# Kernel tuning notes

Hardware: AMD Instinct MI355X
Metric: run time of the kernel (lower is better)

## Reference

```python
import jax, jax.numpy as jnp
import numpy as np
import math

T = 4096          # num tokens (== context_window_len)
IN_SIZE = 2048    # model dim
HEAD_SIZE = 128   # per-head dim


def setup_inputs() -> dict:
    key = jax.random.key(0)
    kx, kq, kk, kv = jax.random.split(key, 4)
    scale = 1.0 / math.sqrt(IN_SIZE)
    x = jax.random.normal(kx, (T, IN_SIZE), dtype=jnp.float32)
    # eqx.nn.Linear(in, out) weight has shape [out, in], applied as W @ x
    Wq = jax.random.normal(kq, (HEAD_SIZE, IN_SIZE), dtype=jnp.float32) * scale
    Wk = jax.random.normal(kk, (HEAD_SIZE, IN_SIZE), dtype=jnp.float32) * scale
    Wv = jax.random.normal(kv, (HEAD_SIZE, IN_SIZE), dtype=jnp.float32) * scale
    return {"x": x, "Wq": Wq, "Wk": Wk, "Wv": Wv}


def reference(x, Wq, Wk, Wv):
    # q, k, v: [T, head_size]
    q = x @ Wq.T
    k = x @ Wk.T
    v = x @ Wv.T
    # scores: [T, T]
    scores = (q @ k.T) / math.sqrt(HEAD_SIZE)
    num_toks = x.shape[0]
    # causal mask: True above the diagonal (masked out)
    causal_mask = ~jnp.tril(jnp.ones((num_toks, num_toks), dtype=bool))
    masked = jnp.where(causal_mask, -jnp.inf, scores)
    attn = jax.nn.softmax(masked, axis=-1)
    return attn @ v
```

## Files before the change

kernel.cpp:

```cpp
#include <hip/hip_runtime.h>
#include <hip/hip_bf16.h>

#define T_TOK 4096
#define D_IN  2048
#define HS    128
#define CKV   4
#define NCH   16

typedef unsigned short u16;
typedef __attribute__((ext_vector_type(8))) __bf16 bf16x8;
typedef __attribute__((ext_vector_type(4))) float f32x4;
typedef __attribute__((ext_vector_type(4))) unsigned short us4;
typedef __attribute__((ext_vector_type(8))) unsigned short us8;

#define GLOBAL_AS __attribute__((address_space(1)))
#define LDS_AS    __attribute__((address_space(3)))

__device__ __forceinline__ void async_ld16(const void* g, void* l) {
  __builtin_amdgcn_global_load_lds((GLOBAL_AS void*)(void*)g, (LDS_AS void*)l, 16, 0, 0);
}

__device__ __forceinline__ u16 f2bf(float v) {
  return __builtin_bit_cast(u16, __float2bfloat16(v));
}

__device__ __forceinline__ void conv_body(const u16* in, u16* out, int n,
                                          int* flag, int write_flag,
                                          int blk, int tid) {
  __shared__ int sflag;
  if (tid < 64) {
    int cnt = 0;
#pragma unroll
    for (int j = 0; j < 8; j++) {
      u16 v = in[(tid * 8 + j) * 2];
      cnt += (((v >> 7) & 0xFF) >= 0xBF) ? 1 : 0;
    }
#pragma unroll
    for (int off = 1; off < 64; off <<= 1) cnt += __shfl_xor(cnt, off);
    if (tid == 0) sflag = (cnt > 8) ? 1 : 0;
  }
  __syncthreads();
  const bool isf32 = (sflag != 0);
  if (tid == 0 && write_flag && blk == 0) *flag = isf32 ? 1 : 0;
  const size_t base = ((size_t)blk * 256 + tid) * 8;
  if (base >= (size_t)n) return;
  if (isf32) {
    const float* f = (const float*)in;
    us4 a, b;
#pragma unroll
    for (int j = 0; j < 4; j++) a[j] = f2bf(f[base + j]);
#pragma unroll
    for (int j = 0; j < 4; j++) b[j] = f2bf(f[base + 4 + j]);
    *(us4*)(out + base) = a;
    *(us4*)(out + base + 4) = b;
  } else {
    *(us8*)(out + base) = *(const us8*)(in + base);
  }
}

__global__ __launch_bounds__(256) void conv_kernel(
    const u16* __restrict__ in, u16* __restrict__ out, int n,
    int* __restrict__ flag) {
  conv_body(in, out, n, flag, 1, blockIdx.x, threadIdx.x);
}

__global__ __launch_bounds__(256) void conv3_kernel(
    const u16* __restrict__ w0, const u16* __restrict__ w1,
    const u16* __restrict__ w2, u16* __restrict__ o0,
    u16* __restrict__ o1, u16* __restrict__ o2) {
  const int mat = blockIdx.x >> 7;
  const int blk = blockIdx.x & 127;
  const u16* in = (mat == 0) ? w0 : ((mat == 1) ? w1 : w2);
  u16* out = (mat == 0) ? o0 : ((mat == 1) ? o1 : o2);
  conv_body(in, out, HS * D_IN, nullptr, 0, blk, threadIdx.x);
}

__global__ __launch_bounds__(256, 2) void qkv_kernel(
    const u16* __restrict__ x, const u16* __restrict__ Wq,
    const u16* __restrict__ Wk, const u16* __restrict__ Wv,
    u16* __restrict__ Q, u16* __restrict__ K, u16* __restrict__ Vt)
{
  __shared__ __align__(16) u16 As[2][64 * 64];
  __shared__ __align__(16) u16 Bs[2][128 * 64];

  const int mat = blockIdx.y;
  const u16* W = (mat == 0) ? Wq : ((mat == 1) ? Wk : Wv);
  const int mtile = blockIdx.x;
  const int tid = threadIdx.x;
  const int wv = tid >> 6, lane = tid & 63, l15 = lane & 15, quad = lane >> 4;
  const int row0 = mtile * 64;

  f32x4 acc[8];
#pragma unroll
  for (int i = 0; i < 8; i++) acc[i] = (f32x4)0.0f;

  auto stage = [&](int k0, int buf) {
#pragma unroll
    for (int j = 0; j < 2; j++) {
      int s = (wv * 2 + j) * 64 + lane;
      int r = s >> 3, cs = s & 7, c = cs ^ (r & 7);
      async_ld16(x + (size_t)(row0 + r) * D_IN + k0 + c * 8,
                 (char*)As[buf] + (size_t)(wv * 2 + j) * 1024);
    }
#pragma unroll
    for (int j = 0; j < 4; j++) {
      int s = (wv * 4 + j) * 64 + lane;
      int n = s >> 3, cs = s & 7, c = cs ^ (n & 7);
      async_ld16(W + (size_t)n * D_IN + k0 + c * 8,
                 (char*)Bs[buf] + (size_t)(wv * 4 + j) * 1024);
    }
  };

  stage(0, 0);
  for (int kt = 0; kt < 32; kt++) {
    const int cur = kt & 1;
    __syncthreads();
    if (kt < 31) stage((kt + 1) * 64, 1 - cur);
#pragma unroll
    for (int kc = 0; kc < 2; kc++) {
      const int rA = 16 * wv + l15;
      const int cl = kc * 4 + quad;
      bf16x8 a = *(const bf16x8*)((const char*)As[cur] + (rA * 8 + (cl ^ (rA & 7))) * 16);
#pragma unroll
      for (int nt = 0; nt < 8; nt++) {
        int n = 16 * nt + l15;
        bf16x8 b = *(const bf16x8*)((const char*)Bs[cur] + (n * 8 + (cl ^ (n & 7))) * 16);
        acc[nt] = __builtin_amdgcn_mfma_f32_16x16x32_bf16(a, b, acc[nt], 0, 0, 0);
      }
    }
  }

  if (mat < 2) {
    u16* out = (mat == 0) ? Q : K;
#pragma unroll
    for (int nt = 0; nt < 8; nt++)
#pragma unroll
      for (int r = 0; r < 4; r++) {
        int m = row0 + 16 * wv + quad * 4 + r;
        int n = 16 * nt + l15;
        out[(size_t)m * HS + n] = f2bf(acc[nt][r]);
      }
  } else {
#pragma unroll
    for (int nt = 0; nt < 8; nt++) {
      int n = 16 * nt + l15;
      int mb = row0 + 16 * wv + quad * 4;
      us4 pk;
#pragma unroll
      for (int r = 0; r < 4; r++) pk[r] = f2bf(acc[nt][r]);
      *(us4*)(Vt + (size_t)n * T_TOK + mb) = pk;
    }
  }
}

__global__ __launch_bounds__(256, 2) void attn_split_kernel(
    const u16* __restrict__ Q, const u16* __restrict__ Kg,
    const u16* __restrict__ Vt, float* __restrict__ Opart,
    float* __restrict__ mstat, float* __restrict__ lstat)
{
  __shared__ __align__(16) u16 Ks[2][64 * 128];
  __shared__ __align__(16) u16 Vs[2][128 * 64];
  __shared__ __align__(16) u16 Ps[4 * 16 * 64];

  const int qtile = 63 - (int)blockIdx.x;
  const int ch = blockIdx.y;
  if (4 * ch > qtile) return;
  const int t0 = 4 * ch;
  const int nsteps = min(CKV, qtile + 1 - t0);
  const int q0 = qtile * 64;
  const int slot = 64 * ch - 2 * ch * (ch - 1) + (qtile - 4 * ch);

  const int tid = threadIdx.x;
  const int wv = tid >> 6, lane = tid & 63, l15 = lane & 15, quad = lane >> 4;

  bf16x8 qf[4];
#pragma unroll
  for (int kc = 0; kc < 4; kc++)
    qf[kc] = *(const bf16x8*)(Q + (size_t)(q0 + 16 * wv + l15) * HS + kc * 32 + quad * 8);

  f32x4 o[8];
#pragma unroll
  for (int i = 0; i < 8; i++) o[i] = (f32x4)0.0f;
  float mrun[4], lrun[4];
#pragma unroll
  for (int r = 0; r < 4; r++) { mrun[r] = -1e30f; lrun[r] = 0.0f; }

  const float sc = 0.12752761571239668f;

  auto stage = [&](int t, int buf) {
#pragma unroll
    for (int j = 0; j < 4; j++) {
      int s = (wv * 4 + j) * 64 + lane;
      int n = s >> 4, cs = s & 15, c = cs ^ (n & 7);
      async_ld16(Kg + (size_t)(t * 64 + n) * HS + c * 8,
                 (char*)Ks[buf] + (size_t)(wv * 4 + j) * 1024);
    }
#pragma unroll
    for (int j = 0; j < 4; j++) {
      int s = (wv * 4 + j) * 64 + lane;
      int vr = s >> 3, cs = s & 7, c = cs ^ (vr & 7);
      async_ld16(Vt + (size_t)vr * T_TOK + t * 64 + c * 8,
                 (char*)Vs[buf] + (size_t)(wv * 4 + j) * 1024);
    }
  };

  stage(t0, 0);
  for (int i = 0; i < nsteps; i++) {
    const int cur = i & 1;
    const int t = t0 + i;
    __syncthreads();
    if (i + 1 < nsteps) stage(t + 1, 1 - cur);

    f32x4 sacc[4];
#pragma unroll
    for (int nt = 0; nt < 4; nt++) sacc[nt] = (f32x4)0.0f;
#pragma unroll
    for (int kc = 0; kc < 4; kc++) {
      const int cl = kc * 4 + quad;
#pragma unroll
      for (int nt = 0; nt < 4; nt++) {
        int n = 16 * nt + l15;
        bf16x8 b = *(const bf16x8*)((const char*)Ks[cur] + (n * 16 + (cl ^ (n & 7))) * 16);
        sacc[nt] = __builtin_amdgcn_mfma_f32_16x16x32_bf16(qf[kc], b, sacc[nt], 0, 0, 0);
      }
    }

    float s2[4][4];
    const bool diag = (t == qtile);
#pragma unroll
    for (int nt = 0; nt < 4; nt++)
#pragma unroll
      for (int r = 0; r < 4; r++) {
        float v = sacc[nt][r] * sc;
        if (diag) {
          int qr = q0 + 16 * wv + quad * 4 + r;
          int kr = t * 64 + 16 * nt + l15;
          if (kr > qr) v = -1e30f;
        }
        s2[nt][r] = v;
      }

    float mnew[4], alpha[4];
#pragma unroll
    for (int r = 0; r < 4; r++) {
      float tmax = fmaxf(fmaxf(s2[0][r], s2[1][r]), fmaxf(s2[2][r], s2[3][r]));
#pragma unroll
      for (int off = 1; off < 16; off <<= 1) tmax = fmaxf(tmax, __shfl_xor(tmax, off));
      mnew[r] = fmaxf(mrun[r], tmax);
      alpha[r] = exp2f(mrun[r] - mnew[r]);
      mrun[r] = mnew[r];
    }
    float p[4][4];
#pragma unroll
    for (int r = 0; r < 4; r++) {
      float s = 0.0f;
#pragma unroll
      for (int nt = 0; nt < 4; nt++) { p[nt][r] = exp2f(s2[nt][r] - mnew[r]); s += p[nt][r]; }
#pragma unroll
      for (int off = 1; off < 16; off <<= 1) s += __shfl_xor(s, off);
      lrun[r] = lrun[r] * alpha[r] + s;
    }
#pragma unroll
    for (int c = 0; c < 8; c++)
#pragma unroll
      for (int r = 0; r < 4; r++) o[c][r] *= alpha[r];

    u16* Pw = Ps + wv * 1024;
#pragma unroll
    for (int nt = 0; nt < 4; nt++)
#pragma unroll
      for (int r = 0; r < 4; r++) {
        int row = quad * 4 + r;
        int col = nt * 16 + l15;
        int cc = col >> 3, wi = col & 7;
        Pw[(row * 8 + (cc ^ (row & 7))) * 8 + wi] = f2bf(p[nt][r]);
      }

#pragma unroll
    for (int kc = 0; kc < 2; kc++) {
      const int cl = kc * 4 + quad;
      bf16x8 a = *(const bf16x8*)((const char*)Pw + (l15 * 8 + (cl ^ (l15 & 7))) * 16);
#pragma unroll
      for (int c = 0; c < 8; c++) {
        int vr = 16 * c + l15;
        bf16x8 b = *(const bf16x8*)((const char*)Vs[cur] + (vr * 8 + (cl ^ (vr & 7))) * 16);
        o[c] = __builtin_amdgcn_mfma_f32_16x16x32_bf16(a, b, o[c], 0, 0, 0);
      }
    }
  }

  float* po = Opart + (size_t)slot * 64 * 128;
#pragma unroll
  for (int c = 0; c < 8; c++)
#pragma unroll
    for (int r = 0; r < 4; r++) {
      int ml = 16 * wv + quad * 4 + r;
      po[ml * 128 + 16 * c + l15] = o[c][r];
    }
  if (l15 == 0) {
#pragma unroll
    for (int r = 0; r < 4; r++) {
      int ml = 16 * wv + quad * 4 + r;
      mstat[slot * 64 + ml] = mrun[r];
      lstat[slot * 64 + ml] = lrun[r];
    }
  }
}

__global__ __launch_bounds__(256) void combine_kernel(
    const float* __restrict__ Opart, const float* __restrict__ mstat,
    const float* __restrict__ lstat, void* __restrict__ out_v,
    const int* __restrict__ dflag)
{
  const int q = blockIdx.x;
  const int cb = blockIdx.y;
  const int tid = threadIdx.x;
  const int row = tid >> 2;
  const int col = cb * 32 + (tid & 3) * 8;
  const int nch = (q + 4) / 4;
  const bool of32 = (*dflag != 0);

  float M = -1e30f;
  {
    int base = 0;
    for (int c = 0; c < nch; c++) {
      int s = base + q - 4 * c;
      M = fmaxf(M, mstat[s * 64 + row]);
      base += 64 - 4 * c;
    }
  }
  float l = 0.0f;
  float acc[8];
#pragma unroll
  for (int j = 0; j < 8; j++) acc[j] = 0.0f;
  {
    int base = 0;
    for (int c = 0; c < nch; c++) {
      int s = base + q - 4 * c;
      float w = exp2f(mstat[s * 64 + row] - M);
      l += w * lstat[s * 64 + row];
      const float* op = Opart + ((size_t)s * 64 + row) * 128 + col;
      f32x4 a = *(const f32x4*)op;
      f32x4 b = *(const f32x4*)(op + 4);
#pragma unroll
      for (int j = 0; j < 4; j++) { acc[j] += w * a[j]; acc[4 + j] += w * b[j]; }
      base += 64 - 4 * c;
    }
  }
  const float inv = 1.0f / l;
  const size_t goff = (size_t)(q * 64 + row) * HS + col;
  if (of32) {
    float* out = (float*)out_v + goff;
    f32x4 r0, r1;
#pragma unroll
    for (int j = 0; j < 4; j++) { r0[j] = acc[j] * inv; r1[j] = acc[4 + j] * inv; }
    *(f32x4*)out = r0;
    *(f32x4*)(out + 4) = r1;
  } else {
    u16* out = (u16*)out_v + goff;
    us4 r0, r1;
#pragma unroll
    for (int j = 0; j < 4; j++) { r0[j] = f2bf(acc[j] * inv); r1[j] = f2bf(acc[4 + j] * inv); }
    *(us4*)out = r0;
    *(us4*)(out + 4) = r1;
  }
}

extern "C" void kernel_launch(void* const* d_in, const int* in_sizes, int n_in,
                              void* d_out, int out_size, void* d_ws, size_t ws_size,
                              hipStream_t stream) {
  const u16* x  = (const u16*)d_in[0];
  const u16* Wq = (const u16*)d_in[1];
  const u16* Wk = (const u16*)d_in[2];
  const u16* Wv = (const u16*)d_in[3];

  u16* xb  = (u16*)d_ws;
  u16* Wqb = xb  + (size_t)T_TOK * D_IN;
  u16* Wkb = Wqb + (size_t)HS * D_IN;
  u16* Wvb = Wkb + (size_t)HS * D_IN;
  u16* Q   = Wvb + (size_t)HS * D_IN;
  u16* K   = Q   + (size_t)T_TOK * HS;
  u16* Vt  = K   + (size_t)T_TOK * HS;
  int* flag = (int*)(Vt + (size_t)T_TOK * HS);

  float* Opart = (float*)d_ws;
  float* mstat = Opart + (size_t)544 * 64 * 128;
  float* lstat = mstat + (size_t)544 * 64;

  const int nx = T_TOK * D_IN;
  conv_kernel<<<nx / 2048, 256, 0, stream>>>(x, xb, nx, flag);
  conv3_kernel<<<384, 256, 0, stream>>>(Wq, Wk, Wv, Wqb, Wkb, Wvb);

  qkv_kernel<<<dim3(64, 3), 256, 0, stream>>>(xb, Wqb, Wkb, Wvb, Q, K, Vt);
  attn_split_kernel<<<dim3(64, NCH), 256, 0, stream>>>(Q, K, Vt, Opart, mstat, lstat);
  combine_kernel<<<dim3(64, 4), 256, 0, stream>>>(Opart, mstat, lstat, d_out, flag);
}
```

Measured before the change: 151.7 us.

## Fuse fp32-to-bf16 conversion of x into the QKV projection kernel

```diff
diff --git a/kernel.cpp b/kernel.cpp
--- a/kernel.cpp
+++ b/kernel.cpp
@@ -24,10 +24,7 @@
   return __builtin_bit_cast(u16, __float2bfloat16(v));
 }
 
-__device__ __forceinline__ void conv_body(const u16* in, u16* out, int n,
-                                          int* flag, int write_flag,
-                                          int blk, int tid) {
-  __shared__ int sflag;
+__device__ __forceinline__ bool detect_f32(const u16* in, int tid, int* sflag) {
   if (tid < 64) {
     int cnt = 0;
 #pragma unroll
@@ -37,13 +34,25 @@
     }
 #pragma unroll
     for (int off = 1; off < 64; off <<= 1) cnt += __shfl_xor(cnt, off);
-    if (tid == 0) sflag = (cnt > 8) ? 1 : 0;
+    if (tid == 0) *sflag = (cnt > 8) ? 1 : 0;
   }
   __syncthreads();
-  const bool isf32 = (sflag != 0);
-  if (tid == 0 && write_flag && blk == 0) *flag = isf32 ? 1 : 0;
+  return (*sflag != 0);
+}
+
+__global__ __launch_bounds__(256) void conv3_kernel(
+    const u16* __restrict__ w0, const u16* __restrict__ w1,
+    const u16* __restrict__ w2, u16* __restrict__ o0,
+    u16* __restrict__ o1, u16* __restrict__ o2, int* __restrict__ flag) {
+  __shared__ int sflag;
+  const int mat = blockIdx.x >> 7;
+  const int blk = blockIdx.x & 127;
+  const u16* in = (mat == 0) ? w0 : ((mat == 1) ? w1 : w2);
+  u16* out = (mat == 0) ? o0 : ((mat == 1) ? o1 : o2);
+  const int tid = threadIdx.x;
+  const bool isf32 = detect_f32(in, tid, &sflag);
+  if (tid == 0 && mat == 0 && blk == 0) *flag = isf32 ? 1 : 0;
   const size_t base = ((size_t)blk * 256 + tid) * 8;
-  if (base >= (size_t)n) return;
   if (isf32) {
     const float* f = (const float*)in;
     us4 a, b;
@@ -56,23 +65,6 @@
   } else {
     *(us8*)(out + base) = *(const us8*)(in + base);
   }
-}
-
-__global__ __launch_bounds__(256) void conv_kernel(
-    const u16* __restrict__ in, u16* __restrict__ out, int n,
-    int* __restrict__ flag) {
-  conv_body(in, out, n, flag, 1, blockIdx.x, threadIdx.x);
-}
-
-__global__ __launch_bounds__(256) void conv3_kernel(
-    const u16* __restrict__ w0, const u16* __restrict__ w1,
-    const u16* __restrict__ w2, u16* __restrict__ o0,
-    u16* __restrict__ o1, u16* __restrict__ o2) {
-  const int mat = blockIdx.x >> 7;
-  const int blk = blockIdx.x & 127;
-  const u16* in = (mat == 0) ? w0 : ((mat == 1) ? w1 : w2);
-  u16* out = (mat == 0) ? o0 : ((mat == 1) ? o1 : o2);
-  conv_body(in, out, HS * D_IN, nullptr, 0, blk, threadIdx.x);
 }
 
 __global__ __launch_bounds__(256, 2) void qkv_kernel(
@@ -82,6 +74,7 @@
 {
   __shared__ __align__(16) u16 As[2][64 * 64];
   __shared__ __align__(16) u16 Bs[2][128 * 64];
+  __shared__ int sflag;
 
   const int mat = blockIdx.y;
   const u16* W = (mat == 0) ? Wq : ((mat == 1) ? Wk : Wv);
@@ -90,11 +83,36 @@
   const int wv = tid >> 6, lane = tid & 63, l15 = lane & 15, quad = lane >> 4;
   const int row0 = mtile * 64;
 
+  const bool isf32 = detect_f32(x, tid, &sflag);
+
   f32x4 acc[8];
 #pragma unroll
   for (int i = 0; i < 8; i++) acc[i] = (f32x4)0.0f;
 
-  auto stage = [&](int k0, int buf) {
+  const int s0 = tid * 2;
+  const int ar = s0 >> 3;
+  const int ac0 = (s0 & 7) ^ (ar & 7);
+  const int ac1 = ((s0 + 1) & 7) ^ (ar & 7);
+
+  f32x4 pa[4];
+  auto loadA_f32 = [&](int k0) {
+    const float* xf = (const float*)x + (size_t)(row0 + ar) * D_IN + k0;
+    pa[0] = *(const f32x4*)(xf + ac0 * 8);
+    pa[1] = *(const f32x4*)(xf + ac0 * 8 + 4);
+    pa[2] = *(const f32x4*)(xf + ac1 * 8);
+    pa[3] = *(const f32x4*)(xf + ac1 * 8 + 4);
+  };
+  auto writeA_f32 = [&](int buf) {
+    us8 c0, c1;
+#pragma unroll
+    for (int j = 0; j < 4; j++) {
+      c0[j] = f2bf(pa[0][j]); c0[4 + j] = f2bf(pa[1][j]);
+      c1[j] = f2bf(pa[2][j]); c1[4 + j] = f2bf(pa[3][j]);
+    }
+    *(us8*)((char*)As[buf] + (size_t)s0 * 16) = c0;
+    *(us8*)((char*)As[buf] + (size_t)(s0 + 1) * 16) = c1;
+  };
+  auto stageA_bf16 = [&](int k0, int buf) {
 #pragma unroll
     for (int j = 0; j < 2; j++) {
       int s = (wv * 2 + j) * 64 + lane;
@@ -102,6 +120,8 @@
       async_ld16(x + (size_t)(row0 + r) * D_IN + k0 + c * 8,
                  (char*)As[buf] + (size_t)(wv * 2 + j) * 1024);
     }
+  };
+  auto stageB = [&](int k0, int buf) {
 #pragma unroll
     for (int j = 0; j < 4; j++) {
       int s = (wv * 4 + j) * 64 + lane;
@@ -111,11 +131,17 @@
     }
   };
 
-  stage(0, 0);
+  stageB(0, 0);
+  if (isf32) loadA_f32(0); else stageA_bf16(0, 0);
+
   for (int kt = 0; kt < 32; kt++) {
     const int cur = kt & 1;
+    if (isf32) writeA_f32(cur);
     __syncthreads();
-    if (kt < 31) stage((kt + 1) * 64, 1 - cur);
+    if (kt < 31) {
+      stageB((kt + 1) * 64, 1 - cur);
+      if (isf32) loadA_f32((kt + 1) * 64); else stageA_bf16((kt + 1) * 64, 1 - cur);
+    }
 #pragma unroll
     for (int kc = 0; kc < 2; kc++) {
       const int rA = 16 * wv + l15;
@@ -374,8 +400,11 @@
   const u16* Wk = (const u16*)d_in[2];
   const u16* Wv = (const u16*)d_in[3];
 
-  u16* xb  = (u16*)d_ws;
-  u16* Wqb = xb  + (size_t)T_TOK * D_IN;
+  float* Opart = (float*)d_ws;
+  float* mstat = Opart + (size_t)544 * 64 * 128;
+  float* lstat = mstat + (size_t)544 * 64;
+
+  u16* Wqb = (u16*)(lstat + (size_t)544 * 64);
   u16* Wkb = Wqb + (size_t)HS * D_IN;
   u16* Wvb = Wkb + (size_t)HS * D_IN;
   u16* Q   = Wvb + (size_t)HS * D_IN;
@@ -383,15 +412,8 @@
   u16* Vt  = K   + (size_t)T_TOK * HS;
   int* flag = (int*)(Vt + (size_t)T_TOK * HS);
 
-  float* Opart = (float*)d_ws;
-  float* mstat = Opart + (size_t)544 * 64 * 128;
-  float* lstat = mstat + (size_t)544 * 64;
-
-  const int nx = T_TOK * D_IN;
-  conv_kernel<<<nx / 2048, 256, 0, stream>>>(x, xb, nx, flag);
-  conv3_kernel<<<384, 256, 0, stream>>>(Wq, Wk, Wv, Wqb, Wkb, Wvb);
-
-  qkv_kernel<<<dim3(64, 3), 256, 0, stream>>>(xb, Wqb, Wkb, Wvb, Q, K, Vt);
+  conv3_kernel<<<384, 256, 0, stream>>>(Wq, Wk, Wv, Wqb, Wkb, Wvb, flag);
+  qkv_kernel<<<dim3(64, 3), 256, 0, stream>>>(x, Wqb, Wkb, Wvb, Q, K, Vt);
   attn_split_kernel<<<dim3(64, NCH), 256, 0, stream>>>(Q, K, Vt, Opart, mstat, lstat);
   combine_kernel<<<dim3(64, 4), 256, 0, stream>>>(Opart, mstat, lstat, d_out, flag);
 }
```

Result: faster. 147.6 us (-2.7%).
